# Optimization experiments

Measured on AMD Instinct MI355X. Metric: run time of the kernel, lower is better.

The kernel has to match this reference:

```python
import jax, jax.numpy as jnp
import numpy as np

B, L, S, D, H, TOPK = 8, 2048, 1000, 1024, 8, 10
E = D // H  # d_keys = 128


def setup_inputs() -> dict:
    key = jax.random.key(0)
    ks = jax.random.split(key, 8)
    s = 1.0 / np.sqrt(D)
    return {
        "target_embedding": jax.random.normal(ks[0], (B, L, D), dtype=jnp.float32),
        "source_embedding": jax.random.normal(ks[1], (S, D), dtype=jnp.float32),
        "Wq": jax.random.normal(ks[2], (D, D), dtype=jnp.float32) * s,
        "bq": jnp.zeros((D,), dtype=jnp.float32),
        "Wk": jax.random.normal(ks[3], (D, D), dtype=jnp.float32) * s,
        "bk": jnp.zeros((D,), dtype=jnp.float32),
        "Wo": jax.random.normal(ks[4], (D, D), dtype=jnp.float32) * s,
        "bo": jnp.zeros((D,), dtype=jnp.float32),
        "data_id": 0,
    }


def reference(target_embedding, source_embedding, Wq, bq, Wk, bk, Wo, bo, data_id):
    # data_id is unused by the original module's math.
    b, l, d = target_embedding.shape
    h, e, topk = H, E, TOPK
    scale = 1.0 / np.sqrt(e)

    q = (target_embedding @ Wq + bq).reshape(b, l, h, e)   # [B,L,H,E]
    k = (source_embedding @ Wk + bk).reshape(-1, h, e)      # [S,H,E]

    scores = jnp.einsum('blhe,she->bhls', q, k)             # [B,H,L,S]
    A = jax.nn.softmax(scale * scores, axis=-1)             # dropout is eval-mode identity
    tmps = A.sum(axis=2)                                    # [B,H,S] head-wise column mass
    _, idxs = jax.lax.top_k(tmps, topk)                     # [B,H,topk]

    kh = jnp.transpose(k, (1, 0, 2))                        # [H,S,E]
    # gather per (batch, head) the topk source key vectors
    tok = kh[jnp.arange(h)[None, :, None], idxs, :]         # [B,H,topk,E]
    tok = jnp.transpose(tok, (0, 2, 1, 3)).reshape(b, topk, h * e)  # [B,topk,D]
    return tok @ Wo + bo                                    # [B,topk,D]
```

## Files before the change

### kernel.cpp

```cpp
#include <hip/hip_runtime.h>
#include <hip/hip_bf16.h>
#include <math.h>

constexpr int B_ = 8;
constexpr int L_ = 2048;
constexpr int S_ = 1000;
constexpr int D_ = 1024;
constexpr int H_ = 8;
constexpr int E_ = 128;
constexpr int TOPK_ = 10;
constexpr float SCALE_LOG2E_ = 0.12751744f;

typedef __attribute__((ext_vector_type(8))) short short8;
typedef __attribute__((ext_vector_type(4))) float f32x4;

__device__ inline unsigned short f2bf(float x) {
    unsigned u = __float_as_uint(x);
    unsigned r = (u + 0x7fffu + ((u >> 16) & 1u)) >> 16;
    return (unsigned short)r;
}
__device__ inline float bf2f(unsigned short s) {
    return __uint_as_float(((unsigned)s) << 16);
}

typedef __attribute__((address_space(1))) const unsigned int gas_u32;
typedef __attribute__((address_space(3))) unsigned int las_u32;
__device__ __forceinline__ void gload_lds16(const void* g, void* l) {
    __builtin_amdgcn_global_load_lds((gas_u32*)g, (las_u32*)l, 16, 0, 0);
}

__global__ __launch_bounds__(256) void gemm_bias_kernel(
    const float* __restrict__ A, const float* __restrict__ Bm,
    const float* __restrict__ bias, float* __restrict__ C,
    int M, int N, int Kd)
{
    __shared__ float As[16][65];
    __shared__ float Bs[16][68];

    const int t  = threadIdx.x;
    const int tx = t & 15;
    const int ty = t >> 4;
    const int m0 = blockIdx.y * 64;
    const int n0 = blockIdx.x * 64;

    float acc[4][4];
#pragma unroll
    for (int i = 0; i < 4; ++i)
#pragma unroll
        for (int j = 0; j < 4; ++j) acc[i][j] = 0.f;

    for (int k0 = 0; k0 < Kd; k0 += 16) {
        {
            const int row = t >> 2;
            const int c4  = (t & 3) * 4;
            float4 v = {0.f, 0.f, 0.f, 0.f};
            if (m0 + row < M)
                v = *(const float4*)&A[(size_t)(m0 + row) * Kd + k0 + c4];
            As[c4 + 0][row] = v.x;
            As[c4 + 1][row] = v.y;
            As[c4 + 2][row] = v.z;
            As[c4 + 3][row] = v.w;
        }
        {
            const int row = t >> 4;
            const int c4  = (t & 15) * 4;
            float4 v = *(const float4*)&Bm[(size_t)(k0 + row) * N + n0 + c4];
            *(float4*)&Bs[row][c4] = v;
        }
        __syncthreads();
#pragma unroll
        for (int k = 0; k < 16; ++k) {
            float a[4], b[4];
#pragma unroll
            for (int i = 0; i < 4; ++i) a[i] = As[k][ty * 4 + i];
            float4 bv = *(const float4*)&Bs[k][tx * 4];
            b[0] = bv.x; b[1] = bv.y; b[2] = bv.z; b[3] = bv.w;
#pragma unroll
            for (int i = 0; i < 4; ++i)
#pragma unroll
                for (int j = 0; j < 4; ++j) acc[i][j] += a[i] * b[j];
        }
        __syncthreads();
    }

#pragma unroll
    for (int i = 0; i < 4; ++i) {
        const int row = m0 + ty * 4 + i;
        if (row < M) {
#pragma unroll
            for (int j = 0; j < 4; ++j) {
                const int col = n0 + tx * 4 + j;
                C[(size_t)row * N + col] = acc[i][j] + bias[col];
            }
        }
    }
}

__global__ __launch_bounds__(256) void splitWT_kernel(
    const float* __restrict__ W,
    unsigned short* __restrict__ WTh, unsigned short* __restrict__ WTl)
{
    __shared__ __attribute__((aligned(16))) float tile[64][68];
    const int t  = threadIdx.x;
    const int k0 = blockIdx.y * 64, n0 = blockIdx.x * 64;
#pragma unroll
    for (int it = 0; it < 4; ++it) {
        int id = it * 256 + t;
        int r = id >> 4, c = id & 15;
        *(float4*)&tile[r][c * 4] = *(const float4*)&W[(size_t)(k0 + r) * D_ + n0 + c * 4];
    }
    __syncthreads();
#pragma unroll
    for (int it = 0; it < 4; ++it) {
        int id = it * 256 + t;
        int n = id >> 4, c = id & 15;
        unsigned short hs[4], ls[4];
#pragma unroll
        for (int i = 0; i < 4; ++i) {
            float x = tile[c * 4 + i][n];
            hs[i] = f2bf(x);
            ls[i] = f2bf(x - bf2f(hs[i]));
        }
        size_t o = (size_t)(n0 + n) * D_ + k0 + c * 4;
        uint2 uh; uh.x = (unsigned)hs[0] | ((unsigned)hs[1] << 16);
                  uh.y = (unsigned)hs[2] | ((unsigned)hs[3] << 16);
        uint2 ul; ul.x = (unsigned)ls[0] | ((unsigned)ls[1] << 16);
                  ul.y = (unsigned)ls[2] | ((unsigned)ls[3] << 16);
        *(uint2*)&WTh[o] = uh;
        *(uint2*)&WTl[o] = ul;
    }
}

__global__ __launch_bounds__(256) void split_src_kernel(
    const float* __restrict__ src,
    unsigned short* __restrict__ Sh, unsigned short* __restrict__ Sl)
{
    int idx  = blockIdx.x * 256 + threadIdx.x;
    int base = idx * 4;
    int row  = base >> 10;
    float4 v = {0.f, 0.f, 0.f, 0.f};
    if (row < S_) v = *(const float4*)&src[base];
    float xs[4] = {v.x, v.y, v.z, v.w};
    unsigned short hs[4], ls[4];
#pragma unroll
    for (int i = 0; i < 4; ++i) {
        hs[i] = f2bf(xs[i]);
        ls[i] = f2bf(xs[i] - bf2f(hs[i]));
    }
    uint2 uh; uh.x = (unsigned)hs[0] | ((unsigned)hs[1] << 16);
              uh.y = (unsigned)hs[2] | ((unsigned)hs[3] << 16);
    uint2 ul; ul.x = (unsigned)ls[0] | ((unsigned)ls[1] << 16);
              ul.y = (unsigned)ls[2] | ((unsigned)ls[3] << 16);
    *(uint2*)&Sh[base] = uh;
    *(uint2*)&Sl[base] = ul;
}

__global__ __launch_bounds__(256, 2) void kproj_kernel(
    const unsigned short* __restrict__ Sh, const unsigned short* __restrict__ Sl,
    const unsigned short* __restrict__ WkTh, const unsigned short* __restrict__ WkTl,
    const float* __restrict__ bk,
    float* __restrict__ Kbuf,
    unsigned short* __restrict__ Kh, unsigned short* __restrict__ Kl)
{
    __shared__ __attribute__((aligned(16))) unsigned short Ah[128 * 64];
    __shared__ __attribute__((aligned(16))) unsigned short Al[128 * 64];
    __shared__ __attribute__((aligned(16))) unsigned short Bh[128 * 64];
    __shared__ __attribute__((aligned(16))) unsigned short Bl[128 * 64];

    const int t    = threadIdx.x;
    const int lane = t & 63, w = t >> 6;
    const int mb   = blockIdx.x >> 3;
    const int n0   = (blockIdx.x & 7) * 128;

    f32x4 acc[2][8];
#pragma unroll
    for (int m = 0; m < 2; ++m)
#pragma unroll
        for (int n = 0; n < 8; ++n) acc[m][n] = (f32x4){0.f, 0.f, 0.f, 0.f};

    for (int k0 = 0; k0 < D_; k0 += 64) {
        __syncthreads();
#pragma unroll
        for (int it = 0; it < 4; ++it) {
            int id = it * 256 + t;
            int r = id >> 3, c = id & 7;
            int lofs = r * 64 + ((c ^ (r & 7)) << 3);
            size_t ga = (size_t)(mb * 128 + r) * D_ + k0 + c * 8;
            *(uint4*)&Ah[lofs] = *(const uint4*)&Sh[ga];
            *(uint4*)&Al[lofs] = *(const uint4*)&Sl[ga];
            size_t gb = (size_t)(n0 + r) * D_ + k0 + c * 8;
            *(uint4*)&Bh[lofs] = *(const uint4*)&WkTh[gb];
            *(uint4*)&Bl[lofs] = *(const uint4*)&WkTl[gb];
        }
        __syncthreads();

#pragma unroll
        for (int ki = 0; ki < 2; ++ki) {
            short8 ah[2], al[2];
#pragma unroll
            for (int m = 0; m < 2; ++m) {
                int r = w * 32 + m * 16 + (lane & 15);
                int slot = ki * 4 + (lane >> 4);
                int lofs = r * 64 + ((slot ^ (r & 7)) << 3);
                ah[m] = *(short8*)&Ah[lofs];
                al[m] = *(short8*)&Al[lofs];
            }
#pragma unroll
            for (int n = 0; n < 8; ++n) {
                int nn = n * 16 + (lane & 15);
                int slot = ki * 4 + (lane >> 4);
                int lofs = nn * 64 + ((slot ^ (nn & 7)) << 3);
                short8 bh = *(short8*)&Bh[lofs];
                short8 bl = *(short8*)&Bl[lofs];
#pragma unroll
                for (int m = 0; m < 2; ++m) {
                    acc[m][n] = __builtin_amdgcn_mfma_f32_16x16x32_bf16(ah[m], bh, acc[m][n], 0, 0, 0);
                    acc[m][n] = __builtin_amdgcn_mfma_f32_16x16x32_bf16(ah[m], bl, acc[m][n], 0, 0, 0);
                    acc[m][n] = __builtin_amdgcn_mfma_f32_16x16x32_bf16(al[m], bh, acc[m][n], 0, 0, 0);
                }
            }
        }
    }

#pragma unroll
    for (int n = 0; n < 8; ++n) {
        int col = n0 + n * 16 + (lane & 15);
        float bkv = bk[col];
#pragma unroll
        for (int m = 0; m < 2; ++m) {
            int rbase = mb * 128 + w * 32 + m * 16 + ((lane >> 4) << 2);
#pragma unroll
            for (int r = 0; r < 4; ++r) {
                int row = rbase + r;
                unsigned short hh = 0, ll = 0;
                if (row < S_) {
                    float kv = acc[m][n][r] + bkv;
                    Kbuf[(size_t)row * D_ + col] = kv;
                    hh = f2bf(kv);
                    ll = f2bf(kv - bf2f(hh));
                }
                Kh[(size_t)row * D_ + col] = hh;
                Kl[(size_t)row * D_ + col] = ll;
            }
        }
    }
}

__global__ __launch_bounds__(256, 2) void qproj_kernel(
    const float* __restrict__ tgt,
    const unsigned short* __restrict__ WqTh, const unsigned short* __restrict__ WqTl,
    const float* __restrict__ bq,
    unsigned short* __restrict__ qhb, unsigned short* __restrict__ qlb)
{
    __shared__ __attribute__((aligned(16))) unsigned short Ah[128 * 64];
    __shared__ __attribute__((aligned(16))) unsigned short Al[128 * 64];
    __shared__ __attribute__((aligned(16))) unsigned short Bh[128 * 64];
    __shared__ __attribute__((aligned(16))) unsigned short Bl[128 * 64];

    const int t    = threadIdx.x;
    const int lane = t & 63, w = t >> 6;
    const int mb   = blockIdx.x >> 3;
    const int n0   = (blockIdx.x & 7) * 128;

    f32x4 acc[2][8];
#pragma unroll
    for (int m = 0; m < 2; ++m)
#pragma unroll
        for (int n = 0; n < 8; ++n) acc[m][n] = (f32x4){0.f, 0.f, 0.f, 0.f};

    for (int k0 = 0; k0 < D_; k0 += 64) {
        __syncthreads();
#pragma unroll
        for (int it = 0; it < 4; ++it) {
            int id = it * 256 + t;
            int r = id >> 3, c = id & 7;
            int lofs = r * 64 + ((c ^ (r & 7)) << 3);
            const float* ga = &tgt[(size_t)(mb * 128 + r) * D_ + k0 + c * 8];
            float4 v0 = *(const float4*)ga;
            float4 v1 = *(const float4*)(ga + 4);
            float xs[8] = {v0.x, v0.y, v0.z, v0.w, v1.x, v1.y, v1.z, v1.w};
            unsigned short hs[8], ls[8];
#pragma unroll
            for (int j = 0; j < 8; ++j) {
                hs[j] = f2bf(xs[j]);
                ls[j] = f2bf(xs[j] - bf2f(hs[j]));
            }
            uint4 uh, ul;
            uh.x = (unsigned)hs[0] | ((unsigned)hs[1] << 16);
            uh.y = (unsigned)hs[2] | ((unsigned)hs[3] << 16);
            uh.z = (unsigned)hs[4] | ((unsigned)hs[5] << 16);
            uh.w = (unsigned)hs[6] | ((unsigned)hs[7] << 16);
            ul.x = (unsigned)ls[0] | ((unsigned)ls[1] << 16);
            ul.y = (unsigned)ls[2] | ((unsigned)ls[3] << 16);
            ul.z = (unsigned)ls[4] | ((unsigned)ls[5] << 16);
            ul.w = (unsigned)ls[6] | ((unsigned)ls[7] << 16);
            *(uint4*)&Ah[lofs] = uh;
            *(uint4*)&Al[lofs] = ul;
            size_t gb = (size_t)(n0 + r) * D_ + k0 + c * 8;
            *(uint4*)&Bh[lofs] = *(const uint4*)&WqTh[gb];
            *(uint4*)&Bl[lofs] = *(const uint4*)&WqTl[gb];
        }
        __syncthreads();

#pragma unroll
        for (int ki = 0; ki < 2; ++ki) {
            short8 ah[2], al[2];
#pragma unroll
            for (int m = 0; m < 2; ++m) {
                int r = w * 32 + m * 16 + (lane & 15);
                int slot = ki * 4 + (lane >> 4);
                int lofs = r * 64 + ((slot ^ (r & 7)) << 3);
                ah[m] = *(short8*)&Ah[lofs];
                al[m] = *(short8*)&Al[lofs];
            }
#pragma unroll
            for (int n = 0; n < 8; ++n) {
                int nn = n * 16 + (lane & 15);
                int slot = ki * 4 + (lane >> 4);
                int lofs = nn * 64 + ((slot ^ (nn & 7)) << 3);
                short8 bh = *(short8*)&Bh[lofs];
                short8 bl = *(short8*)&Bl[lofs];
#pragma unroll
                for (int m = 0; m < 2; ++m) {
                    acc[m][n] = __builtin_amdgcn_mfma_f32_16x16x32_bf16(ah[m], bh, acc[m][n], 0, 0, 0);
                    acc[m][n] = __builtin_amdgcn_mfma_f32_16x16x32_bf16(ah[m], bl, acc[m][n], 0, 0, 0);
                    acc[m][n] = __builtin_amdgcn_mfma_f32_16x16x32_bf16(al[m], bh, acc[m][n], 0, 0, 0);
                }
            }
        }
    }

#pragma unroll
    for (int n = 0; n < 8; ++n) {
        int col = n0 + n * 16 + (lane & 15);
        float bqv = bq[col];
#pragma unroll
        for (int m = 0; m < 2; ++m) {
            int rbase = mb * 128 + w * 32 + m * 16 + ((lane >> 4) << 2);
#pragma unroll
            for (int r = 0; r < 4; ++r) {
                float q = (acc[m][n][r] + bqv) * SCALE_LOG2E_;
                unsigned short hh = f2bf(q);
                qhb[(size_t)(rbase + r) * D_ + col] = hh;
                qlb[(size_t)(rbase + r) * D_ + col] = f2bf(q - bf2f(hh));
            }
        }
    }
}

__global__ __launch_bounds__(256, 2) void scores2p_kernel(
    const unsigned short* __restrict__ qhb, const unsigned short* __restrict__ qlb,
    const unsigned short* __restrict__ Kh, const unsigned short* __restrict__ Kl,
    float* __restrict__ tmps, int b0)
{
    __shared__ __attribute__((aligned(16))) unsigned short SH[2][64 * 128];
    __shared__ __attribute__((aligned(16))) unsigned short SL[2][64 * 128];
    __shared__ float tmps_l[1024];

    const int t    = threadIdx.x;
    const int lane = t & 63, w = t >> 6;
    const int blk  = blockIdx.x;
    const int bb   = blk >> 7;
    const int h    = (blk >> 4) & 7;
    const int lt   = blk & 15;
    const int qrow0 = bb * L_ + lt * 128;
    const int bh_i  = (b0 + bb) * H_ + h;
    const int kr0   = t >> 4;
    const int kc0   = t & 15;

    for (int i = t; i < 1024; i += 256) tmps_l[i] = 0.f;

#define SC_ISSUE(ST, BUF)                                                   \
    do {                                                                    \
        _Pragma("unroll")                                                   \
        for (int it = 0; it < 4; ++it) {                                    \
            int r = it * 16 + kr0;                                          \
            size_t g = (size_t)((ST) * 64 + r) * D_ + h * E_                \
                       + ((kc0 ^ (r & 15)) << 3);                           \
            int lofs = it * 4096 + t * 16;      \
            gload_lds16(&Kh[g], (char*)&SH[(BUF)][0] + lofs);               \
            gload_lds16(&Kl[g], (char*)&SL[(BUF)][0] + lofs);               \
        }                                                                   \
    } while (0)

    SC_ISSUE(0, 1);

    short8 qh[2][4], ql[2][4];
#pragma unroll
    for (int hf = 0; hf < 2; ++hf) {
        __syncthreads();
#pragma unroll
        for (int it = 0; it < 4; ++it) {
            int r = it * 16 + kr0;
            size_t g = (size_t)(qrow0 + hf * 64 + r) * D_ + h * E_ + kc0 * 8;
            int lofs = r * 128 + ((kc0 ^ (r & 15)) << 3);
            *(uint4*)&SH[0][lofs] = *(const uint4*)&qhb[g];
            *(uint4*)&SL[0][lofs] = *(const uint4*)&qlb[g];
        }
        __syncthreads();
        if ((w >> 1) == hf) {
#pragma unroll
            for (int rg = 0; rg < 2; ++rg)
#pragma unroll
                for (int ki = 0; ki < 4; ++ki) {
                    int rq = (w & 1) * 32 + rg * 16 + (lane & 15);
                    int slot = ki * 4 + (lane >> 4);
                    int lofs = rq * 128 + ((slot ^ (rq & 15)) << 3);
                    qh[rg][ki] = *(short8*)&SH[0][lofs];
                    ql[rg][ki] = *(short8*)&SL[0][lofs];
                }
        }
    }

    float zacc[2][4];
#pragma unroll
    for (int rg = 0; rg < 2; ++rg)
#pragma unroll
        for (int r = 0; r < 4; ++r) zacc[rg][r] = 0.f;
    float invZ[2][4];

    int cur = 1;
    for (int u = 0; u < 32; ++u) {
        const int st = u & 15;
        __syncthreads();
        if (u < 31) SC_ISSUE((u + 1) & 15, cur ^ 1);

        f32x4 acc[2][4];
#pragma unroll
        for (int rg = 0; rg < 2; ++rg)
#pragma unroll
            for (int nf = 0; nf < 4; ++nf) acc[rg][nf] = (f32x4){0.f, 0.f, 0.f, 0.f};

#pragma unroll
        for (int ki = 0; ki < 4; ++ki)
#pragma unroll
            for (int nf = 0; nf < 4; ++nf) {
                int sr = nf * 16 + (lane & 15);
                int slot = ki * 4 + (lane >> 4);
                int lofs = sr * 128 + ((slot ^ (sr & 15)) << 3);
                short8 bh = *(short8*)&SH[cur][lofs];
                short8 bl = *(short8*)&SL[cur][lofs];
#pragma unroll
                for (int rg = 0; rg < 2; ++rg) {
                    acc[rg][nf] = __builtin_amdgcn_mfma_f32_16x16x32_bf16(qh[rg][ki], bh, acc[rg][nf], 0, 0, 0);
                    acc[rg][nf] = __builtin_amdgcn_mfma_f32_16x16x32_bf16(qh[rg][ki], bl, acc[rg][nf], 0, 0, 0);
                    acc[rg][nf] = __builtin_amdgcn_mfma_f32_16x16x32_bf16(ql[rg][ki], bh, acc[rg][nf], 0, 0, 0);
                }
            }

        if (u < 16) {
#pragma unroll
            for (int nf = 0; nf < 4; ++nf) {
                int s = st * 64 + nf * 16 + (lane & 15);
                if (s < S_) {
#pragma unroll
                    for (int rg = 0; rg < 2; ++rg)
#pragma unroll
                        for (int r = 0; r < 4; ++r)
                            zacc[rg][r] += exp2f(acc[rg][nf][r]);
                }
            }
            if (u == 15) {
#pragma unroll
                for (int rg = 0; rg < 2; ++rg)
#pragma unroll
                    for (int r = 0; r < 4; ++r) {
                        float z = zacc[rg][r];
                        z += __shfl_xor(z, 1);
                        z += __shfl_xor(z, 2);
                        z += __shfl_xor(z, 4);
                        z += __shfl_xor(z, 8);
                        invZ[rg][r] = 1.f / z;
                    }
            }
        } else {
#pragma unroll
            for (int nf = 0; nf < 4; ++nf) {
                int s = st * 64 + nf * 16 + (lane & 15);
                if (s < S_) {
                    float val = 0.f;
#pragma unroll
                    for (int rg = 0; rg < 2; ++rg)
#pragma unroll
                        for (int r = 0; r < 4; ++r)
                            val += exp2f(acc[rg][nf][r]) * invZ[rg][r];
                    atomicAdd(&tmps_l[s], val);
                }
            }
        }
        cur ^= 1;
    }
#undef SC_ISSUE

    __syncthreads();
    for (int i = t; i < S_; i += 256)
        atomicAdd(&tmps[(size_t)bh_i * S_ + i], tmps_l[i]);
}

__global__ __launch_bounds__(256) void topk_kernel(
    const float* __restrict__ tmps, int* __restrict__ idxs)
{
    const int bh = blockIdx.x;
    const int t  = threadIdx.x;
    __shared__ float v[S_];
    __shared__ float rv[256];
    __shared__ int   ri[256];

    for (int i = t; i < S_; i += 256) v[i] = tmps[(size_t)bh * S_ + i];
    __syncthreads();

    for (int it = 0; it < TOPK_; ++it) {
        float best = -1e38f;
        int bi = 0x7fffffff;
        for (int s = t; s < S_; s += 256) {
            const float x = v[s];
            if (x > best) { best = x; bi = s; }
        }
        rv[t] = best; ri[t] = bi;
        __syncthreads();
        for (int k = 128; k > 0; k >>= 1) {
            if (t < k) {
                const float x = rv[t + k];
                const int  xi = ri[t + k];
                if (x > rv[t] || (x == rv[t] && xi < ri[t])) { rv[t] = x; ri[t] = xi; }
            }
            __syncthreads();
        }
        if (t == 0) {
            idxs[bh * TOPK_ + it] = ri[0];
            v[ri[0]] = -1e38f;
        }
        __syncthreads();
    }
}

__global__ __launch_bounds__(256) void gather_kernel(
    const float* __restrict__ K, const int* __restrict__ idxs,
    float* __restrict__ tok)
{
    const int o = blockIdx.x * 256 + threadIdx.x;
    if (o >= B_ * TOPK_ * D_) return;
    const int d  = o & (D_ - 1);
    const int tt = (o >> 10) % TOPK_;
    const int b  = o / (D_ * TOPK_);
    const int h  = d >> 7;
    const int s  = idxs[(b * H_ + h) * TOPK_ + tt];
    tok[o] = K[(size_t)s * D_ + d];
}

extern "C" void kernel_launch(void* const* d_in, const int* in_sizes, int n_in,
                              void* d_out, int out_size, void* d_ws, size_t ws_size,
                              hipStream_t stream)
{
    const float* tgt = (const float*)d_in[0];
    const float* src = (const float*)d_in[1];
    const float* Wq  = (const float*)d_in[2];
    const float* bq  = (const float*)d_in[3];
    const float* Wk  = (const float*)d_in[4];
    const float* bk  = (const float*)d_in[5];
    const float* Wo  = (const float*)d_in[6];
    const float* bo  = (const float*)d_in[7];
    float* out = (float*)d_out;

    char* ws = (char*)d_ws;
    size_t off = 0;
    float*          Kbuf = (float*)(ws + off);          off += (size_t)S_ * D_ * 4;
    float*          tmps = (float*)(ws + off);          off += (size_t)B_ * H_ * S_ * 4;
    int*            idxs = (int*)(ws + off);            off += (size_t)B_ * H_ * TOPK_ * 4;
    off = (off + 255) & ~(size_t)255;
    float*          tok  = (float*)(ws + off);          off += (size_t)B_ * TOPK_ * D_ * 4;
    unsigned short* Kh   = (unsigned short*)(ws + off); off += (size_t)1024 * D_ * 2;
    unsigned short* Kl   = (unsigned short*)(ws + off); off += (size_t)1024 * D_ * 2;
    unsigned short* WqTh = (unsigned short*)(ws + off); off += (size_t)D_ * D_ * 2;
    unsigned short* WqTl = (unsigned short*)(ws + off); off += (size_t)D_ * D_ * 2;
    unsigned short* WkTh = (unsigned short*)(ws + off); off += (size_t)D_ * D_ * 2;
    unsigned short* WkTl = (unsigned short*)(ws + off); off += (size_t)D_ * D_ * 2;
    unsigned short* Sh   = (unsigned short*)(ws + off); off += (size_t)1024 * D_ * 2;
    unsigned short* Sl   = (unsigned short*)(ws + off); off += (size_t)1024 * D_ * 2;
    unsigned short* qhb  = (unsigned short*)(ws + off);
    const size_t fixed_bytes = off;
    const size_t q_plane_b = (size_t)L_ * D_ * 2;

    int nb_fit = 1;
    if (ws_size > fixed_bytes) {
        size_t f = (ws_size - fixed_bytes) / (2 * q_plane_b);
        nb_fit = (f < 1) ? 1 : (f > 8 ? 8 : (int)f);
    }

    hipMemsetAsync(tmps, 0, (size_t)B_ * H_ * S_ * sizeof(float), stream);

    split_src_kernel<<<(1024 * D_) / (256 * 4), 256, 0, stream>>>(src, Sh, Sl);
    {
        dim3 g(D_ / 64, D_ / 64);
        splitWT_kernel<<<g, 256, 0, stream>>>(Wq, WqTh, WqTl);
        splitWT_kernel<<<g, 256, 0, stream>>>(Wk, WkTh, WkTl);
    }

    kproj_kernel<<<64, 256, 0, stream>>>(Sh, Sl, WkTh, WkTl, bk, Kbuf, Kh, Kl);

    for (int b0 = 0; b0 < B_; b0 += nb_fit) {
        int nb = (B_ - b0 < nb_fit) ? (B_ - b0) : nb_fit;
        unsigned short* qlb = qhb + (size_t)nb_fit * q_plane_b / 2;
        qproj_kernel<<<nb * 128, 256, 0, stream>>>(
            tgt + (size_t)b0 * L_ * D_, WqTh, WqTl, bq, qhb, qlb);
        scores2p_kernel<<<nb * 128, 256, 0, stream>>>(qhb, qlb, Kh, Kl, tmps, b0);
    }

    topk_kernel<<<B_ * H_, 256, 0, stream>>>(tmps, idxs);
    gather_kernel<<<(B_ * TOPK_ * D_ + 255) / 256, 256, 0, stream>>>(Kbuf, idxs, tok);
    {
        dim3 g(D_ / 64, (B_ * TOPK_ + 63) / 64);
        gemm_bias_kernel<<<g, 256, 0, stream>>>(tok, Wo, bo, out, B_ * TOPK_, D_, D_);
    }
}
```

Baseline: 472.7 us.

## Use direct global-to-LDS loads in projections, shrink score tiles, fast exp2

The K and Q projection GEMMs now stage their weight (and, for K, input) tiles with global_load_lds, swizzling on the global side instead of going through registers. The scores kernel halves its source-key tile from 64 to 32 rows, so each of the 4 waves now holds its own 32 query rows and the loop runs 64 steps; launch bounds are raised to 4 blocks per CU to increase occupancy. exp2f is replaced by the hardware exp2 builtin and the bf16 split uses the HIP conversion intrinsics. Smaller tiles double the number of barriers and K reloads per block in exchange for lower LDS use and higher occupancy.

```diff
diff --git a/kernel.cpp b/kernel.cpp
--- a/kernel.cpp
+++ b/kernel.cpp
@@ -21,6 +21,14 @@
 }
 __device__ inline float bf2f(unsigned short s) {
     return __uint_as_float(((unsigned)s) << 16);
+}
+
+__device__ __forceinline__ float fexp2(float x) {
+#if __has_builtin(__builtin_amdgcn_exp2f)
+    return __builtin_amdgcn_exp2f(x);
+#else
+    return __expf(x * 0.69314718056f);
+#endif
 }
 
 typedef __attribute__((address_space(1))) const unsigned int gas_u32;
@@ -182,15 +190,13 @@
         __syncthreads();
 #pragma unroll
         for (int it = 0; it < 4; ++it) {
-            int id = it * 256 + t;
-            int r = id >> 3, c = id & 7;
-            int lofs = r * 64 + ((c ^ (r & 7)) << 3);
-            size_t ga = (size_t)(mb * 128 + r) * D_ + k0 + c * 8;
-            *(uint4*)&Ah[lofs] = *(const uint4*)&Sh[ga];
-            *(uint4*)&Al[lofs] = *(const uint4*)&Sl[ga];
-            size_t gb = (size_t)(n0 + r) * D_ + k0 + c * 8;
-            *(uint4*)&Bh[lofs] = *(const uint4*)&WkTh[gb];
-            *(uint4*)&Bl[lofs] = *(const uint4*)&WkTl[gb];
+            int r = it * 32 + (t >> 3), c = t & 7;
+            size_t gofs = (size_t)r * D_ + k0 + ((c ^ (r & 7)) << 3);
+            int db = it * 4096 + t * 16;
+            gload_lds16(&Sh[(size_t)(mb * 128) * D_ + gofs], (char*)Ah + db);
+            gload_lds16(&Sl[(size_t)(mb * 128) * D_ + gofs], (char*)Al + db);
+            gload_lds16(&WkTh[(size_t)n0 * D_ + gofs], (char*)Bh + db);
+            gload_lds16(&WkTl[(size_t)n0 * D_ + gofs], (char*)Bl + db);
         }
         __syncthreads();
 
@@ -272,6 +278,14 @@
         __syncthreads();
 #pragma unroll
         for (int it = 0; it < 4; ++it) {
+            int r = it * 32 + (t >> 3), c = t & 7;
+            size_t gb = (size_t)(n0 + r) * D_ + k0 + ((c ^ (r & 7)) << 3);
+            int db = it * 4096 + t * 16;
+            gload_lds16(&WqTh[gb], (char*)Bh + db);
+            gload_lds16(&WqTl[gb], (char*)Bl + db);
+        }
+#pragma unroll
+        for (int it = 0; it < 4; ++it) {
             int id = it * 256 + t;
             int r = id >> 3, c = id & 7;
             int lofs = r * 64 + ((c ^ (r & 7)) << 3);
@@ -282,8 +296,10 @@
             unsigned short hs[8], ls[8];
 #pragma unroll
             for (int j = 0; j < 8; ++j) {
-                hs[j] = f2bf(xs[j]);
-                ls[j] = f2bf(xs[j] - bf2f(hs[j]));
+                __hip_bfloat16 hb = __float2bfloat16(xs[j]);
+                hs[j] = *(unsigned short*)&hb;
+                __hip_bfloat16 lb = __float2bfloat16(xs[j] - __bfloat162float(hb));
+                ls[j] = *(unsigned short*)&lb;
             }
             uint4 uh, ul;
             uh.x = (unsigned)hs[0] | ((unsigned)hs[1] << 16);
@@ -296,9 +312,6 @@
             ul.w = (unsigned)ls[6] | ((unsigned)ls[7] << 16);
             *(uint4*)&Ah[lofs] = uh;
             *(uint4*)&Al[lofs] = ul;
-            size_t gb = (size_t)(n0 + r) * D_ + k0 + c * 8;
-            *(uint4*)&Bh[lofs] = *(const uint4*)&WqTh[gb];
-            *(uint4*)&Bl[lofs] = *(const uint4*)&WqTl[gb];
         }
         __syncthreads();
 
@@ -348,13 +361,13 @@
     }
 }
 
-__global__ __launch_bounds__(256, 2) void scores2p_kernel(
+__global__ __launch_bounds__(256, 4) void scores2p_kernel(
     const unsigned short* __restrict__ qhb, const unsigned short* __restrict__ qlb,
     const unsigned short* __restrict__ Kh, const unsigned short* __restrict__ Kl,
     float* __restrict__ tmps, int b0)
 {
-    __shared__ __attribute__((aligned(16))) unsigned short SH[2][64 * 128];
-    __shared__ __attribute__((aligned(16))) unsigned short SL[2][64 * 128];
+    __shared__ __attribute__((aligned(16))) unsigned short SH[2][32 * 128];
+    __shared__ __attribute__((aligned(16))) unsigned short SL[2][32 * 128];
     __shared__ float tmps_l[1024];
 
     const int t    = threadIdx.x;
@@ -373,13 +386,13 @@
 #define SC_ISSUE(ST, BUF)                                                   \
     do {                                                                    \
         _Pragma("unroll")                                                   \
-        for (int it = 0; it < 4; ++it) {                                    \
+        for (int it = 0; it < 2; ++it) {                                    \
             int r = it * 16 + kr0;                                          \
-            size_t g = (size_t)((ST) * 64 + r) * D_ + h * E_                \
+            size_t g = (size_t)((ST) * 32 + r) * D_ + h * E_                \
                        + ((kc0 ^ (r & 15)) << 3);                           \
-            int lofs = it * 4096 + t * 16;      \
-            gload_lds16(&Kh[g], (char*)&SH[(BUF)][0] + lofs);               \
-            gload_lds16(&Kl[g], (char*)&SL[(BUF)][0] + lofs);               \
+            int db = it * 4096 + t * 16;                                    \
+            gload_lds16(&Kh[g], (char*)&SH[(BUF)][0] + db);                 \
+            gload_lds16(&Kl[g], (char*)&SL[(BUF)][0] + db);                 \
         }                                                                   \
     } while (0)
 
@@ -387,23 +400,23 @@
 
     short8 qh[2][4], ql[2][4];
 #pragma unroll
-    for (int hf = 0; hf < 2; ++hf) {
-        __syncthreads();
-#pragma unroll
-        for (int it = 0; it < 4; ++it) {
+    for (int ch = 0; ch < 4; ++ch) {
+        __syncthreads();
+#pragma unroll
+        for (int it = 0; it < 2; ++it) {
             int r = it * 16 + kr0;
-            size_t g = (size_t)(qrow0 + hf * 64 + r) * D_ + h * E_ + kc0 * 8;
+            size_t g = (size_t)(qrow0 + ch * 32 + r) * D_ + h * E_ + kc0 * 8;
             int lofs = r * 128 + ((kc0 ^ (r & 15)) << 3);
             *(uint4*)&SH[0][lofs] = *(const uint4*)&qhb[g];
             *(uint4*)&SL[0][lofs] = *(const uint4*)&qlb[g];
         }
         __syncthreads();
-        if ((w >> 1) == hf) {
+        if (w == ch) {
 #pragma unroll
             for (int rg = 0; rg < 2; ++rg)
 #pragma unroll
                 for (int ki = 0; ki < 4; ++ki) {
-                    int rq = (w & 1) * 32 + rg * 16 + (lane & 15);
+                    int rq = rg * 16 + (lane & 15);
                     int slot = ki * 4 + (lane >> 4);
                     int lofs = rq * 128 + ((slot ^ (rq & 15)) << 3);
                     qh[rg][ki] = *(short8*)&SH[0][lofs];
@@ -420,21 +433,21 @@
     float invZ[2][4];
 
     int cur = 1;
-    for (int u = 0; u < 32; ++u) {
-        const int st = u & 15;
-        __syncthreads();
-        if (u < 31) SC_ISSUE((u + 1) & 15, cur ^ 1);
-
-        f32x4 acc[2][4];
+    for (int u = 0; u < 64; ++u) {
+        const int st = u & 31;
+        __syncthreads();
+        if (u < 63) SC_ISSUE((u + 1) & 31, cur ^ 1);
+
+        f32x4 acc[2][2];
 #pragma unroll
         for (int rg = 0; rg < 2; ++rg)
 #pragma unroll
-            for (int nf = 0; nf < 4; ++nf) acc[rg][nf] = (f32x4){0.f, 0.f, 0.f, 0.f};
+            for (int nf = 0; nf < 2; ++nf) acc[rg][nf] = (f32x4){0.f, 0.f, 0.f, 0.f};
 
 #pragma unroll
         for (int ki = 0; ki < 4; ++ki)
 #pragma unroll
-            for (int nf = 0; nf < 4; ++nf) {
+            for (int nf = 0; nf < 2; ++nf) {
                 int sr = nf * 16 + (lane & 15);
                 int slot = ki * 4 + (lane >> 4);
                 int lofs = sr * 128 + ((slot ^ (sr & 15)) << 3);
@@ -448,19 +461,19 @@
                 }
             }
 
-        if (u < 16) {
-#pragma unroll
-            for (int nf = 0; nf < 4; ++nf) {
-                int s = st * 64 + nf * 16 + (lane & 15);
+        if (u < 32) {
+#pragma unroll
+            for (int nf = 0; nf < 2; ++nf) {
+                int s = st * 32 + nf * 16 + (lane & 15);
                 if (s < S_) {
 #pragma unroll
                     for (int rg = 0; rg < 2; ++rg)
 #pragma unroll
                         for (int r = 0; r < 4; ++r)
-                            zacc[rg][r] += exp2f(acc[rg][nf][r]);
+                            zacc[rg][r] += fexp2(acc[rg][nf][r]);
                 }
             }
-            if (u == 15) {
+            if (u == 31) {
 #pragma unroll
                 for (int rg = 0; rg < 2; ++rg)
 #pragma unroll
@@ -475,15 +488,15 @@
             }
         } else {
 #pragma unroll
-            for (int nf = 0; nf < 4; ++nf) {
-                int s = st * 64 + nf * 16 + (lane & 15);
+            for (int nf = 0; nf < 2; ++nf) {
+                int s = st * 32 + nf * 16 + (lane & 15);
                 if (s < S_) {
                     float val = 0.f;
 #pragma unroll
                     for (int rg = 0; rg < 2; ++rg)
 #pragma unroll
                         for (int r = 0; r < 4; ++r)
-                            val += exp2f(acc[rg][nf][r]) * invZ[rg][r];
+                            val += fexp2(acc[rg][nf][r]) * invZ[rg][r];
                     atomicAdd(&tmps_l[s], val);
                 }
             }
```

New measurement: 447.7 us. 5.3% less time.
